# Optimization experiments

Hardware: AMD Instinct MI355X
Metric: run time of the kernel (lower is better)

The kernel has to match this reference:

```python
import jax, jax.numpy as jnp
import numpy as np

EMBED_DIM = 512
NUM_HEADS = 8
HEAD_DIM = EMBED_DIM // NUM_HEADS


def setup_inputs() -> dict:
    key = jax.random.key(0)
    k1, k2, k3, k4, k5, k6 = jax.random.split(key, 6)
    B, S, D = 2, 4096, EMBED_DIM
    scale = 1.0 / np.sqrt(D)
    return {
        "inputs": jax.random.normal(k1, (B, S, D), dtype=jnp.float32),
        "Wq": jax.random.normal(k2, (D, D), dtype=jnp.float32) * scale,
        "Wk": jax.random.normal(k3, (D, D), dtype=jnp.float32) * scale,
        "Wv": jax.random.normal(k4, (D, D), dtype=jnp.float32) * scale,
        "Wc": jax.random.normal(k5, (D, D), dtype=jnp.float32) * scale,
        "bc": jax.random.normal(k6, (D,), dtype=jnp.float32) * 0.01,
    }


def reference(inputs, Wq, Wk, Wv, Wc, bc):
    B, S, D = inputs.shape
    H, Hd = NUM_HEADS, HEAD_DIM

    def split_heads(x):
        # [B,S,D] -> [B,H,S,Hd]
        return x.reshape(B, S, H, Hd).transpose(0, 2, 1, 3)

    # nn.Linear applies x @ W.T
    q = split_heads(inputs @ Wq.T).astype(jnp.float32)
    k = split_heads(inputs @ Wk.T).astype(jnp.float32)
    v = split_heads(inputs @ Wv.T).astype(jnp.float32)

    scores = jnp.einsum("bhqd,bhkd->bhqk", q, k) / np.sqrt(Hd).astype(jnp.float32)
    weights = jax.nn.softmax(scores, axis=-1)
    attended = jnp.einsum("bhqk,bhkd->bhqd", weights, v).astype(inputs.dtype)
    attended = attended.transpose(0, 2, 1, 3).reshape(B, S, D)
    return attended @ Wc.T + bc
```

## Files before the change

### kernel.cpp

```cpp
#include <hip/hip_runtime.h>
#include <cstdint>
#include <cstddef>

typedef _Float16 half_t;
typedef half_t h8 __attribute__((ext_vector_type(8)));
typedef half_t h4 __attribute__((ext_vector_type(4)));
typedef float f4 __attribute__((ext_vector_type(4)));
typedef float f16v __attribute__((ext_vector_type(16)));
typedef unsigned int u32;

static constexpr int S_LEN  = 4096;
static constexpr int DMODEL = 512;
static constexpr int NH     = 8;
static constexpr int HD     = 64;
static constexpr int BATCH  = 2;
static constexpr int MTOK   = BATCH * S_LEN;

#define QSCALE 0.18033688011112043f

__device__ __forceinline__ void g2lds16(const void* g, void* l) {
    __builtin_amdgcn_global_load_lds(
        (const __attribute__((address_space(1))) u32*)(uintptr_t)g,
        (__attribute__((address_space(3))) u32*)(u32)(uintptr_t)l,
        16, 0, 0);
}

__device__ __forceinline__ f4 mfma16(h8 a, h8 b, f4 c) {
    return __builtin_amdgcn_mfma_f32_16x16x32_f16(a, b, c, 0, 0, 0);
}

__device__ __forceinline__ f16v mfma32(h8 a, h8 b, f16v c) {
    return __builtin_amdgcn_mfma_f32_32x32x16_f16(a, b, c, 0, 0, 0);
}

__device__ __forceinline__ u32 pkrtz(float a, float b) {
#if __has_builtin(__builtin_amdgcn_cvt_pkrtz)
    auto r = __builtin_amdgcn_cvt_pkrtz(a, b);
    return __builtin_bit_cast(u32, r);
#else
    union { half_t h[2]; u32 u; } x;
    x.h[0] = (half_t)a; x.h[1] = (half_t)b;
    return x.u;
#endif
}

__device__ __forceinline__ void plswap(u32 a, u32 b, u32& lo, u32& hi_, int hi) {
#if __has_builtin(__builtin_amdgcn_permlane32_swap)
    auto r = __builtin_amdgcn_permlane32_swap(a, b, false, false);
    lo = (u32)r[0]; hi_ = (u32)r[1];
#else
    u32 ta = __shfl_xor(a, 32);
    u32 tb = __shfl_xor(b, 32);
    lo  = hi ? tb : a;
    hi_ = hi ? b  : ta;
#endif
}

__global__ void cvt_all(const float* __restrict__ X,
                        const float* __restrict__ w0, const float* __restrict__ w1,
                        const float* __restrict__ w2, const float* __restrict__ w3,
                        half_t* __restrict__ Xh,
                        half_t* __restrict__ o0, half_t* __restrict__ o1,
                        half_t* __restrict__ o2, half_t* __restrict__ o3) {
    int bx = blockIdx.x;
    const float* in;
    half_t* out;
    float s = 1.0f;
    int i;
    if (bx < 2048) {
        in = X; out = Xh;
        i = (bx * 256 + threadIdx.x) * 8;
    } else {
        int y = (bx - 2048) >> 7;
        in  = (y==0) ? w0 : (y==1) ? w1 : (y==2) ? w2 : w3;
        out = (y==0) ? o0 : (y==1) ? o1 : (y==2) ? o2 : o3;
        if (y == 0) s = QSCALE;
        i = (((bx - 2048) & 127) * 256 + threadIdx.x) * 8;
    }
    const float4* p = (const float4*)(in + i);
    float4 a = p[0], b = p[1];
    h8 h;
    h[0]=(half_t)(a.x*s); h[1]=(half_t)(a.y*s); h[2]=(half_t)(a.z*s); h[3]=(half_t)(a.w*s);
    h[4]=(half_t)(b.x*s); h[5]=(half_t)(b.y*s); h[6]=(half_t)(b.z*s); h[7]=(half_t)(b.w*s);
    *(h8*)(out + i) = h;
}

__device__ __forceinline__ void gemm_core4(const half_t* __restrict__ A,
                                           const half_t* __restrict__ B,
                                           int m0, int n0, int Kdim,
                                           half_t* As, half_t* Bs,
                                           f4 (&acc)[4][4]) {
    const int tid  = threadIdx.x;
    const int lane = tid & 63;
    const int w    = tid >> 6;
    const int quad = lane >> 4;
    const int low  = lane & 15;
    const int wr   = (w >> 1) * 64;
    const int wc   = (w & 1) * 64;

    f4 zero = {0.f, 0.f, 0.f, 0.f};
    #pragma unroll
    for (int i = 0; i < 4; ++i)
        #pragma unroll
        for (int j = 0; j < 4; ++j) acc[i][j] = zero;

    auto stage = [&](int kk, int p) {
        #pragma unroll
        for (int it = 0; it < 2; ++it) {
            int c = tid + 256 * it;
            int row = c >> 2, cs = c & 3;
            int gc = cs ^ ((row >> 1) & 3);
            g2lds16(A + (size_t)(m0 + row) * Kdim + kk + gc * 8, As + p * 4096 + c * 8);
        }
        #pragma unroll
        for (int it = 0; it < 2; ++it) {
            int c = tid + 256 * it;
            int row = c >> 2, cs = c & 3;
            int gc = cs ^ ((row >> 1) & 3);
            g2lds16(B + (size_t)(n0 + row) * Kdim + kk + gc * 8, Bs + p * 4096 + c * 8);
        }
    };

    stage(0, 0);
    const int T = Kdim / 32;
    for (int t = 0; t < T; ++t) {
        __syncthreads();
        if (t + 1 < T) stage((t + 1) * 32, (t + 1) & 1);

        const half_t* Ac = As + (t & 1) * 4096;
        const half_t* Bc = Bs + (t & 1) * 4096;
        h8 af[4], bf[4];
        #pragma unroll
        for (int i = 0; i < 4; ++i) {
            int r = wr + i * 16 + low;
            af[i] = *(const h8*)(Ac + r * 32 + (quad ^ ((r >> 1) & 3)) * 8);
        }
        #pragma unroll
        for (int j = 0; j < 4; ++j) {
            int r = wc + j * 16 + low;
            bf[j] = *(const h8*)(Bc + r * 32 + (quad ^ ((r >> 1) & 3)) * 8);
        }
        #pragma unroll
        for (int i = 0; i < 4; ++i)
            #pragma unroll
            for (int j = 0; j < 4; ++j)
                acc[i][j] = mfma16(af[i], bf[j], acc[i][j]);
    }
}

__global__ __launch_bounds__(256, 3) void gemm_proj(
    const half_t* __restrict__ X,
    const half_t* __restrict__ Wq, const half_t* __restrict__ Wk, const half_t* __restrict__ Wv,
    half_t* __restrict__ Q, half_t* __restrict__ K, half_t* __restrict__ Vt) {
    __shared__ half_t SM[16384];
    const int z  = blockIdx.z;
    const int bx = blockIdx.x;

    const half_t *A, *B;
    int m0, n0;
    if (z < 2) {
        A = X; B = (z == 0) ? Wq : Wk;
        m0 = (bx >> 2) * 128; n0 = (bx & 3) * 128;
    } else {
        A = Wv; B = X;
        m0 = (bx & 3) * 128; n0 = (bx >> 2) * 128;
    }
    f4 acc[4][4];
    gemm_core4(A, B, m0, n0, DMODEL, SM, SM + 8192, acc);

    const int tid  = threadIdx.x;
    const int lane = tid & 63;
    const int w    = tid >> 6;
    const int quad = lane >> 4, low = lane & 15;
    const int wr = (w >> 1) * 64, wc = (w & 1) * 64;

    __syncthreads();
    #pragma unroll
    for (int i = 0; i < 4; ++i) {
        #pragma unroll
        for (int j = 0; j < 4; ++j) {
            int coln = wc + j * 16 + low;
            #pragma unroll
            for (int r = 0; r < 4; ++r) {
                int row  = wr + i * 16 + quad * 4 + r;
                int sblk = (coln >> 3) ^ (((row >> 2) & 3) << 1);
                SM[row * 128 + sblk * 8 + (coln & 7)] = (half_t)acc[i][j][r];
            }
        }
    }
    __syncthreads();

    if (z < 2) {
        half_t* O = (z == 0) ? Q : K;
        #pragma unroll
        for (int it = 0; it < 8; ++it) {
            int c = tid + 256 * it;
            int row = c >> 4, blk = c & 15;
            h8 v = *(const h8*)(SM + row * 128 + (blk ^ (((row >> 2) & 3) << 1)) * 8);
            int m = m0 + row, n = n0 + blk * 8;
            int h = n >> 6, d = n & 63;
            int b = m >> 12, s = m & 4095;
            *(h8*)(O + (((size_t)(b * NH + h) << 12) + s) * 64 + d) = v;
        }
    } else {
        #pragma unroll
        for (int it = 0; it < 8; ++it) {
            int c = tid + 256 * it;
            int row = c >> 4, blk = c & 15;
            h8 v = *(const h8*)(SM + row * 128 + (blk ^ (((row >> 2) & 3) << 1)) * 8);
            int dg = m0 + row, tok = n0 + blk * 8;
            int b = tok >> 12, s = tok & 4095;
            *(h8*)(Vt + (((size_t)(b * NH + (dg >> 6))) << 18) + ((size_t)(dg & 63) << 12) + s) = v;
        }
    }
}

__global__ __launch_bounds__(256, 3) void gemm_out(
    const half_t* __restrict__ A, const half_t* __restrict__ W,
    const float* __restrict__ bias, float* __restrict__ out) {
    __shared__ half_t As[2 * 128 * 32];
    __shared__ half_t Bs[2 * 128 * 32];
    const int bx = blockIdx.x;
    const int m0 = (bx >> 2) * 128;
    const int n0 = (bx & 3) * 128;
    f4 acc[4][4];
    gemm_core4(A, W, m0, n0, DMODEL, As, Bs, acc);

    const int lane = threadIdx.x & 63;
    const int w    = threadIdx.x >> 6;
    const int quad = lane >> 4, low = lane & 15;
    const int wr = (w >> 1) * 64, wc = (w & 1) * 64;

    #pragma unroll
    for (int i = 0; i < 4; ++i) {
        int mb = m0 + wr + i * 16 + quad * 4;
        #pragma unroll
        for (int j = 0; j < 4; ++j) {
            int n = n0 + wc + j * 16 + low;
            float bv = bias[n];
            #pragma unroll
            for (int r = 0; r < 4; ++r)
                out[(size_t)(mb + r) * DMODEL + n] = acc[i][j][r] + bv;
        }
    }
}

__global__ __launch_bounds__(256, 2) void flash_attn(
    const half_t* __restrict__ Q,
    const half_t* __restrict__ K,
    const half_t* __restrict__ V,
    half_t* __restrict__ Oa) {
    __shared__ half_t Ks[2][128 * 64];
    __shared__ half_t Vs[2][64 * 128];

    const int tid  = threadIdx.x;
    const int lane = tid & 63;
    const int w    = tid >> 6;
    const int l31  = lane & 31;
    const int hi   = lane >> 5;
    const int bh   = blockIdx.y;
    const int q0   = blockIdx.x * 128 + w * 32;

    const half_t* Qb = Q + ((size_t)bh << 18);
    const half_t* Kb = K + ((size_t)bh << 18);
    const half_t* Vb = V + ((size_t)bh << 18);

    h8 qf[4];
    #pragma unroll
    for (int ks = 0; ks < 4; ++ks)
        qf[ks] = *(const h8*)(Qb + (size_t)(q0 + l31) * 64 + ks * 16 + hi * 8);

    f16v zz;
    #pragma unroll
    for (int r = 0; r < 16; ++r) zz[r] = 0.f;

    f16v Oacc[2];
    Oacc[0] = zz; Oacc[1] = zz;
    f4 rs = {0.f, 0.f, 0.f, 0.f};

    auto stage = [&](int k0, int p) {
        #pragma unroll
        for (int it = 0; it < 4; ++it) {
            int c = tid + 256 * it;
            int key = k0 + (c >> 8) * 32 + l31;
            int col = ((c >> 6) & 3) * 16 + hi * 8;
            g2lds16(Kb + (size_t)key * 64 + col, &Ks[p][c * 8]);
        }
        #pragma unroll
        for (int it = 0; it < 4; ++it) {
            int c = tid + 256 * it;
            int d   = (c >> 9) * 32 + l31;
            int key = k0 + ((c >> 6) & 7) * 16 + hi * 8;
            g2lds16(Vb + (size_t)d * S_LEN + key, &Vs[p][c * 8]);
        }
    };

    stage(0, 0);

    for (int c = 0; c < S_LEN / 128; ++c) {
        __syncthreads();
        if (c + 1 < S_LEN / 128) stage((c + 1) * 128, (c + 1) & 1);

        const half_t* Kl = Ks[c & 1] + lane * 8;
        const half_t* Vl = Vs[c & 1] + lane * 8;

        f16v sc[4];
        #pragma unroll
        for (int nt = 0; nt < 4; ++nt) {
            #pragma unroll
            for (int ks = 0; ks < 4; ++ks) {
                h8 kf = *(const h8*)(Kl + nt * 2048 + ks * 512);
                sc[nt] = mfma32(kf, qf[ks], ks == 0 ? zz : sc[nt]);
            }
        }

        #pragma unroll
        for (int nt = 0; nt < 4; ++nt) {
            float p[16];
            #pragma unroll
            for (int r = 0; r < 16; ++r) {
                p[r] = __builtin_amdgcn_exp2f(sc[nt][r]);
                rs[r & 3] += p[r];
            }
            u32 a0 = pkrtz(p[0],  p[1]);
            u32 a1 = pkrtz(p[2],  p[3]);
            u32 a2 = pkrtz(p[4],  p[5]);
            u32 a3 = pkrtz(p[6],  p[7]);
            u32 a4 = pkrtz(p[8],  p[9]);
            u32 a5 = pkrtz(p[10], p[11]);
            u32 a6 = pkrtz(p[12], p[13]);
            u32 a7 = pkrtz(p[14], p[15]);

            union H8U { u32 u[4]; h8 v; } b0, b1;
            plswap(a0, a2, b0.u[0], b0.u[2], hi);
            plswap(a1, a3, b0.u[1], b0.u[3], hi);
            plswap(a4, a6, b1.u[0], b1.u[2], hi);
            plswap(a5, a7, b1.u[1], b1.u[3], hi);

            #pragma unroll
            for (int dt = 0; dt < 2; ++dt) {
                h8 vf0 = *(const h8*)(Vl + dt * 4096 + (nt * 2 + 0) * 512);
                h8 vf1 = *(const h8*)(Vl + dt * 4096 + (nt * 2 + 1) * 512);
                Oacc[dt] = mfma32(vf0, b0.v, Oacc[dt]);
                Oacc[dt] = mfma32(vf1, b1.v, Oacc[dt]);
            }
        }
    }

    float lsum = (rs[0] + rs[1]) + (rs[2] + rs[3]);
    lsum += __shfl_xor(lsum, 32);
    float inv = 1.0f / lsum;

    const int b = bh >> 3, h = bh & 7;
    half_t* Ob = Oa + ((size_t)(b * S_LEN + q0 + l31)) * DMODEL + h * 64;
    #pragma unroll
    for (int dt = 0; dt < 2; ++dt)
        #pragma unroll
        for (int rg = 0; rg < 4; ++rg) {
            h4 o;
            #pragma unroll
            for (int e = 0; e < 4; ++e) o[e] = (half_t)(Oacc[dt][rg * 4 + e] * inv);
            *(h4*)(Ob + dt * 32 + rg * 8 + hi * 4) = o;
        }
}

extern "C" void kernel_launch(void* const* d_in, const int* in_sizes, int n_in,
                              void* d_out, int out_size, void* d_ws, size_t ws_size,
                              hipStream_t stream) {
    const float* X  = (const float*)d_in[0];
    const float* Wq = (const float*)d_in[1];
    const float* Wk = (const float*)d_in[2];
    const float* Wv = (const float*)d_in[3];
    const float* Wc = (const float*)d_in[4];
    const float* bc = (const float*)d_in[5];
    float* out = (float*)d_out;

    char* ws = (char*)d_ws;
    const size_t SZ_X = (size_t)MTOK * DMODEL * 2;
    const size_t SZ_W = (size_t)DMODEL * DMODEL * 2;
    half_t* Xh   = (half_t*)(ws);
    half_t* Wqh  = (half_t*)(ws + SZ_X);
    half_t* Wkh  = (half_t*)(ws + SZ_X + SZ_W);
    half_t* Wvh  = (half_t*)(ws + SZ_X + 2 * SZ_W);
    half_t* Wch  = (half_t*)(ws + SZ_X + 3 * SZ_W);
    half_t* Qh   = (half_t*)(ws + SZ_X + 4 * SZ_W);
    half_t* Kh   = (half_t*)(ws + 2 * SZ_X + 4 * SZ_W);
    half_t* Vt   = (half_t*)(ws + 3 * SZ_X + 4 * SZ_W);
    half_t* Att  = (half_t*)(ws + 4 * SZ_X + 4 * SZ_W);

    cvt_all<<<2048 + 512, 256, 0, stream>>>(X, Wq, Wk, Wv, Wc, Xh, Wqh, Wkh, Wvh, Wch);
    gemm_proj<<<dim3(256, 1, 3), 256, 0, stream>>>(Xh, Wqh, Wkh, Wvh, Qh, Kh, Vt);
    flash_attn<<<dim3(32, 16), 256, 0, stream>>>(Qh, Kh, Vt, Att);
    gemm_out<<<256, 256, 0, stream>>>(Att, Wch, bc, out);
}
```

Measured before the change: 191.2 us.

## Split KV range across two blocks with atomic fp32 partial outputs and combine pass

```diff
diff --git a/kernel.cpp b/kernel.cpp
--- a/kernel.cpp
+++ b/kernel.cpp
@@ -15,6 +15,7 @@
 static constexpr int HD     = 64;
 static constexpr int BATCH  = 2;
 static constexpr int MTOK   = BATCH * S_LEN;
+static constexpr size_t OHEAD = (size_t)S_LEN * HD;
 
 #define QSCALE 0.18033688011112043f
 
@@ -245,11 +246,21 @@
     }
 }
 
-__global__ __launch_bounds__(256, 2) void flash_attn(
+__global__ __launch_bounds__(256) void zero_ol(float* A9, float* B7, float* Lp) {
+    int i = blockIdx.x * 256 + threadIdx.x;
+    float4 z = {0.f, 0.f, 0.f, 0.f};
+    if (i < 589824)            ((float4*)A9)[i] = z;
+    else if (i < 1048576)      ((float4*)B7)[i - 589824] = z;
+    else if (i < 1064960)      ((float4*)Lp)[i - 1048576] = z;
+}
+
+__global__ __launch_bounds__(512, 4) void flash_attn(
     const half_t* __restrict__ Q,
     const half_t* __restrict__ K,
     const half_t* __restrict__ V,
-    half_t* __restrict__ Oa) {
+    float* __restrict__ OA9,
+    float* __restrict__ OB7,
+    float* __restrict__ Lp) {
     __shared__ half_t Ks[2][128 * 64];
     __shared__ half_t Vs[2][64 * 128];
 
@@ -259,7 +270,9 @@
     const int l31  = lane & 31;
     const int hi   = lane >> 5;
     const int bh   = blockIdx.y;
-    const int q0   = blockIdx.x * 128 + w * 32;
+    const int kvh  = blockIdx.z;
+    const int q0   = blockIdx.x * 256 + w * 32;
+    const int kbase = kvh * 2048;
 
     const half_t* Qb = Q + ((size_t)bh << 18);
     const half_t* Kb = K + ((size_t)bh << 18);
@@ -280,26 +293,26 @@
 
     auto stage = [&](int k0, int p) {
         #pragma unroll
-        for (int it = 0; it < 4; ++it) {
-            int c = tid + 256 * it;
-            int key = k0 + (c >> 8) * 32 + l31;
-            int col = ((c >> 6) & 3) * 16 + hi * 8;
+        for (int i2 = 0; i2 < 2; ++i2) {
+            int c = tid + 512 * i2;
+            int key = k0 + (c >> 8) * 32 + (c & 31);
+            int col = ((c >> 6) & 3) * 16 + ((c >> 5) & 1) * 8;
             g2lds16(Kb + (size_t)key * 64 + col, &Ks[p][c * 8]);
         }
         #pragma unroll
-        for (int it = 0; it < 4; ++it) {
-            int c = tid + 256 * it;
-            int d   = (c >> 9) * 32 + l31;
-            int key = k0 + ((c >> 6) & 7) * 16 + hi * 8;
+        for (int i2 = 0; i2 < 2; ++i2) {
+            int c = tid + 512 * i2;
+            int d   = (c >> 9) * 32 + (c & 31);
+            int key = k0 + ((c >> 6) & 7) * 16 + ((c >> 5) & 1) * 8;
             g2lds16(Vb + (size_t)d * S_LEN + key, &Vs[p][c * 8]);
         }
     };
 
-    stage(0, 0);
-
-    for (int c = 0; c < S_LEN / 128; ++c) {
+    stage(kbase, 0);
+
+    for (int c = 0; c < 16; ++c) {
         __syncthreads();
-        if (c + 1 < S_LEN / 128) stage((c + 1) * 128, (c + 1) & 1);
+        if (c + 1 < 16) stage(kbase + (c + 1) * 128, (c + 1) & 1);
 
         const half_t* Kl = Ks[c & 1] + lane * 8;
         const half_t* Vl = Vs[c & 1] + lane * 8;
@@ -349,19 +362,36 @@
 
     float lsum = (rs[0] + rs[1]) + (rs[2] + rs[3]);
     lsum += __shfl_xor(lsum, 32);
-    float inv = 1.0f / lsum;
-
-    const int b = bh >> 3, h = bh & 7;
-    half_t* Ob = Oa + ((size_t)(b * S_LEN + q0 + l31)) * DMODEL + h * 64;
+
+    float* Ob = ((bh < 9) ? OA9 + (size_t)bh * OHEAD
+                          : OB7 + (size_t)(bh - 9) * OHEAD)
+                + (size_t)(q0 + l31) * 64;
     #pragma unroll
     for (int dt = 0; dt < 2; ++dt)
         #pragma unroll
-        for (int rg = 0; rg < 4; ++rg) {
-            h4 o;
-            #pragma unroll
-            for (int e = 0; e < 4; ++e) o[e] = (half_t)(Oacc[dt][rg * 4 + e] * inv);
-            *(h4*)(Ob + dt * 32 + rg * 8 + hi * 4) = o;
-        }
+        for (int rg = 0; rg < 4; ++rg)
+            #pragma unroll
+            for (int e = 0; e < 4; ++e)
+                atomicAdd(Ob + dt * 32 + rg * 8 + hi * 4 + e, Oacc[dt][rg * 4 + e]);
+    if (hi == 0)
+        atomicAdd(Lp + bh * S_LEN + q0 + l31, lsum);
+}
+
+__global__ __launch_bounds__(256) void combine_o(
+    const float* __restrict__ OA9, const float* __restrict__ OB7,
+    const float* __restrict__ Lp, half_t* __restrict__ AttQ) {
+    size_t e0 = ((size_t)blockIdx.x * 256 + threadIdx.x) * 8;
+    size_t row = e0 >> 6;
+    int d0 = (int)(e0 & 63);
+    int bh = (int)(row >> 12), q = (int)(row & 4095);
+    const float* Ob = ((bh < 9) ? OA9 + (size_t)bh * OHEAD
+                                : OB7 + (size_t)(bh - 9) * OHEAD)
+                      + (size_t)q * 64 + d0;
+    float inv = 1.0f / Lp[row];
+    h8 o;
+    #pragma unroll
+    for (int e = 0; e < 8; ++e) o[e] = (half_t)(Ob[e] * inv);
+    *(h8*)(AttQ + ((size_t)((bh >> 3) * S_LEN + q)) * DMODEL + (bh & 7) * 64 + d0) = o;
 }
 
 extern "C" void kernel_launch(void* const* d_in, const int* in_sizes, int n_in,
@@ -386,10 +416,14 @@
     half_t* Qh   = (half_t*)(ws + SZ_X + 4 * SZ_W);
     half_t* Kh   = (half_t*)(ws + 2 * SZ_X + 4 * SZ_W);
     half_t* Vt   = (half_t*)(ws + 3 * SZ_X + 4 * SZ_W);
-    half_t* Att  = (half_t*)(ws + 4 * SZ_X + 4 * SZ_W);
+    float*  OA9  = (float*)(ws);
+    float*  OB7  = (float*)(ws + 4 * SZ_X + 4 * SZ_W);
+    float*  Lp   = OB7 + 7 * OHEAD;
 
     cvt_all<<<2048 + 512, 256, 0, stream>>>(X, Wq, Wk, Wv, Wc, Xh, Wqh, Wkh, Wvh, Wch);
     gemm_proj<<<dim3(256, 1, 3), 256, 0, stream>>>(Xh, Wqh, Wkh, Wvh, Qh, Kh, Vt);
-    flash_attn<<<dim3(32, 16), 256, 0, stream>>>(Qh, Kh, Vt, Att);
-    gemm_out<<<256, 256, 0, stream>>>(Att, Wch, bc, out);
-}
+    zero_ol<<<4160, 256, 0, stream>>>(OA9, OB7, Lp);
+    flash_attn<<<dim3(16, 16, 2), 512, 0, stream>>>(Qh, Kh, Vt, OA9, OB7, Lp);
+    combine_o<<<2048, 256, 0, stream>>>(OA9, OB7, Lp, Qh);
+    gemm_out<<<256, 256, 0, stream>>>(Qh, Wch, bc, out);
+}
```

New measurement: 393.2 us. +105.6%, slower.

## Split attention over two KV halves and merge partial outputs in combine kernel

Applied to the files above, without the earlier changes.

```diff
diff --git a/kernel.cpp b/kernel.cpp
--- a/kernel.cpp
+++ b/kernel.cpp
@@ -15,6 +15,7 @@
 static constexpr int HD     = 64;
 static constexpr int BATCH  = 2;
 static constexpr int MTOK   = BATCH * S_LEN;
+static constexpr size_t LP  = (size_t)16 * 4096;
 
 #define QSCALE 0.18033688011112043f
 
@@ -245,13 +246,15 @@
     }
 }
 
-__global__ __launch_bounds__(256, 2) void flash_attn(
+__global__ __launch_bounds__(256, 4) void flash_attn(
     const half_t* __restrict__ Q,
     const half_t* __restrict__ K,
     const half_t* __restrict__ V,
-    half_t* __restrict__ Oa) {
-    __shared__ half_t Ks[2][128 * 64];
-    __shared__ half_t Vs[2][64 * 128];
+    half_t* __restrict__ O0,
+    half_t* __restrict__ O1,
+    float* __restrict__ Lp) {
+    __shared__ half_t Ks[128 * 64];
+    __shared__ half_t Vs[64 * 128];
 
     const int tid  = threadIdx.x;
     const int lane = tid & 63;
@@ -259,7 +262,9 @@
     const int l31  = lane & 31;
     const int hi   = lane >> 5;
     const int bh   = blockIdx.y;
+    const int kvh  = blockIdx.z;
     const int q0   = blockIdx.x * 128 + w * 32;
+    const int kbase = kvh * 2048;
 
     const half_t* Qb = Q + ((size_t)bh << 18);
     const half_t* Kb = K + ((size_t)bh << 18);
@@ -278,31 +283,30 @@
     Oacc[0] = zz; Oacc[1] = zz;
     f4 rs = {0.f, 0.f, 0.f, 0.f};
 
-    auto stage = [&](int k0, int p) {
+    auto stage = [&](int k0) {
         #pragma unroll
         for (int it = 0; it < 4; ++it) {
             int c = tid + 256 * it;
             int key = k0 + (c >> 8) * 32 + l31;
             int col = ((c >> 6) & 3) * 16 + hi * 8;
-            g2lds16(Kb + (size_t)key * 64 + col, &Ks[p][c * 8]);
+            g2lds16(Kb + (size_t)key * 64 + col, &Ks[c * 8]);
         }
         #pragma unroll
         for (int it = 0; it < 4; ++it) {
             int c = tid + 256 * it;
             int d   = (c >> 9) * 32 + l31;
             int key = k0 + ((c >> 6) & 7) * 16 + hi * 8;
-            g2lds16(Vb + (size_t)d * S_LEN + key, &Vs[p][c * 8]);
+            g2lds16(Vb + (size_t)d * S_LEN + key, &Vs[c * 8]);
         }
     };
 
-    stage(0, 0);
-
-    for (int c = 0; c < S_LEN / 128; ++c) {
+    stage(kbase);
+
+    for (int c = 0; c < 16; ++c) {
         __syncthreads();
-        if (c + 1 < S_LEN / 128) stage((c + 1) * 128, (c + 1) & 1);
-
-        const half_t* Kl = Ks[c & 1] + lane * 8;
-        const half_t* Vl = Vs[c & 1] + lane * 8;
+
+        const half_t* Kl = Ks + lane * 8;
+        const half_t* Vl = Vs + lane * 8;
 
         f16v sc[4];
         #pragma unroll
@@ -345,14 +349,16 @@
                 Oacc[dt] = mfma32(vf1, b1.v, Oacc[dt]);
             }
         }
+
+        __syncthreads();
+        if (c + 1 < 16) stage(kbase + (c + 1) * 128);
     }
 
     float lsum = (rs[0] + rs[1]) + (rs[2] + rs[3]);
     lsum += __shfl_xor(lsum, 32);
     float inv = 1.0f / lsum;
 
-    const int b = bh >> 3, h = bh & 7;
-    half_t* Ob = Oa + ((size_t)(b * S_LEN + q0 + l31)) * DMODEL + h * 64;
+    half_t* Ob = (kvh ? O1 : O0) + ((size_t)bh * S_LEN + q0 + l31) * 64;
     #pragma unroll
     for (int dt = 0; dt < 2; ++dt)
         #pragma unroll
@@ -362,6 +368,27 @@
             for (int e = 0; e < 4; ++e) o[e] = (half_t)(Oacc[dt][rg * 4 + e] * inv);
             *(h4*)(Ob + dt * 32 + rg * 8 + hi * 4) = o;
         }
+    if (hi == 0)
+        Lp[(size_t)kvh * LP + (size_t)bh * S_LEN + q0 + l31] = lsum;
+}
+
+__global__ __launch_bounds__(256) void combine_o(
+    const half_t* __restrict__ O0, const half_t* __restrict__ O1,
+    const float* __restrict__ Lp, half_t* __restrict__ Att) {
+    size_t e0 = ((size_t)blockIdx.x * 256 + threadIdx.x) * 8;
+    size_t row = e0 >> 6;
+    int d0 = (int)(e0 & 63);
+    float l0 = Lp[row], l1 = Lp[LP + row];
+    float inv = 1.0f / (l0 + l1);
+    float w0 = l0 * inv, w1 = l1 * inv;
+    h8 a = *(const h8*)(O0 + e0);
+    h8 b = *(const h8*)(O1 + e0);
+    h8 o;
+    #pragma unroll
+    for (int e = 0; e < 8; ++e)
+        o[e] = (half_t)((float)a[e] * w0 + (float)b[e] * w1);
+    int bh = (int)(row >> 12), q = (int)(row & 4095);
+    *(h8*)(Att + ((size_t)((bh >> 3) * S_LEN + q)) * DMODEL + (bh & 7) * 64 + d0) = o;
 }
 
 extern "C" void kernel_launch(void* const* d_in, const int* in_sizes, int n_in,
@@ -379,17 +406,20 @@
     const size_t SZ_X = (size_t)MTOK * DMODEL * 2;
     const size_t SZ_W = (size_t)DMODEL * DMODEL * 2;
     half_t* Xh   = (half_t*)(ws);
+    half_t* Op0  = (half_t*)(ws);
     half_t* Wqh  = (half_t*)(ws + SZ_X);
+    float*  Lp   = (float*) (ws + SZ_X);
     half_t* Wkh  = (half_t*)(ws + SZ_X + SZ_W);
     half_t* Wvh  = (half_t*)(ws + SZ_X + 2 * SZ_W);
     half_t* Wch  = (half_t*)(ws + SZ_X + 3 * SZ_W);
     half_t* Qh   = (half_t*)(ws + SZ_X + 4 * SZ_W);
     half_t* Kh   = (half_t*)(ws + 2 * SZ_X + 4 * SZ_W);
     half_t* Vt   = (half_t*)(ws + 3 * SZ_X + 4 * SZ_W);
-    half_t* Att  = (half_t*)(ws + 4 * SZ_X + 4 * SZ_W);
+    half_t* Op1  = (half_t*)(ws + 4 * SZ_X + 4 * SZ_W);
 
     cvt_all<<<2048 + 512, 256, 0, stream>>>(X, Wq, Wk, Wv, Wc, Xh, Wqh, Wkh, Wvh, Wch);
     gemm_proj<<<dim3(256, 1, 3), 256, 0, stream>>>(Xh, Wqh, Wkh, Wvh, Qh, Kh, Vt);
-    flash_attn<<<dim3(32, 16), 256, 0, stream>>>(Qh, Kh, Vt, Att);
-    gemm_out<<<256, 256, 0, stream>>>(Att, Wch, bc, out);
-}
+    flash_attn<<<dim3(32, 16, 2), 256, 0, stream>>>(Qh, Kh, Vt, Op0, Op1, Lp);
+    combine_o<<<2048, 256, 0, stream>>>(Op0, Op1, Lp, Qh);
+    gemm_out<<<256, 256, 0, stream>>>(Qh, Wch, bc, out);
+}
```

New measurement: 249.2 us. 1.3x slower.
